# Kernel optimization log

Measured on AMD Instinct MI355X. Metric: run time of the kernel, lower is better.

The kernel has to match this reference:

```python
import jax, jax.numpy as jnp
import numpy as np

B, C, H, W = 8, 512, 32, 32
N = H * W
FG_THRES, BG_THRES, TOPK = 0.7, 0.6, 12


def setup_inputs() -> dict:
    key = jax.random.key(0)
    k1, k2, k3 = jax.random.split(key, 3)
    feature_q = jax.random.normal(k1, (B, C, H, W), dtype=jnp.float32)
    support_feat = jax.random.normal(k2, (B, C, H, W), dtype=jnp.float32)
    support_mask = jax.random.randint(k3, (B, H, W), 0, 2).astype(jnp.int32)
    return {"feature_q": feature_q, "support_feat": support_feat, "support_mask": support_mask}


def _masked_avg_pool(feat, mask):
    # feat [B,C,H,W], mask [B,1,H,W]; interpolate to same size is identity
    return jnp.sum(feat * mask, axis=(2, 3)) / (jnp.sum(mask, axis=(2, 3)) + 1e-5)


def _cosine(a, b):
    # F.cosine_similarity along channel dim 1 (eps=1e-8), with broadcasting
    dot = jnp.sum(a * b, axis=1)
    na = jnp.sqrt(jnp.sum(a * a, axis=1))
    nb = jnp.sqrt(jnp.sum(b * b, axis=1))
    return dot / jnp.maximum(na * nb, 1e-8)


def _similarity(feature_q, fg_proto, bg_proto):
    sim_fg = _cosine(feature_q, fg_proto)
    sim_bg = _cosine(feature_q, bg_proto)
    return jnp.stack([sim_bg, sim_fg], axis=1) * 10.0  # [B,2,H,W]


def _select_weights(pred, thres):
    # pred [N] -> float {0,1} selection weights; threshold mask, topk-12 fallback
    m = pred > thres
    _, top_idx = jax.lax.top_k(pred, TOPK)
    tm = jnp.zeros_like(m).at[top_idx].set(True)
    return jnp.where(m.sum() > 0, m, tm).astype(pred.dtype)


def _ssp_single(cur_feat, pred_fg, pred_bg):
    # cur_feat [C,N]; masked formulation == torch's variable-length column select
    wf = _select_weights(pred_fg, FG_THRES)
    wb = _select_weights(pred_bg, BG_THRES)
    fg_proto = jnp.sum(cur_feat * wf, axis=-1) / wf.sum()  # [C]
    bg_proto = jnp.sum(cur_feat * wb, axis=-1) / wb.sum()
    cn = cur_feat / jnp.sqrt(jnp.sum(cur_feat * cur_feat, axis=0, keepdims=True))
    sim = (cn.T @ cn) * 2.0  # [N,N] cosine sim, scaled
    neg = jnp.asarray(-1e30, sim.dtype)
    fg_attn = jax.nn.softmax(jnp.where(wf[None, :] > 0, sim, neg), axis=-1)
    bg_attn = jax.nn.softmax(jnp.where(wb[None, :] > 0, sim, neg), axis=-1)
    fg_local = (fg_attn @ cur_feat.T).T  # [C,N]
    bg_local = (bg_attn @ cur_feat.T).T
    return fg_proto, bg_proto, fg_local, bg_local


def reference(feature_q, support_feat, support_mask):
    mask_f = (support_mask == 1).astype(feature_q.dtype)[:, None]  # [B,1,H,W]
    mask_b = (support_mask == 0).astype(feature_q.dtype)[:, None]
    FP = _masked_avg_pool(support_feat, mask_f)[:, :, None, None]  # [B,C,1,1]
    BP = _masked_avg_pool(support_feat, mask_b)[:, :, None, None]
    out_0 = _similarity(feature_q, FP, BP)  # [B,2,H,W]
    pred = jax.nn.softmax(out_0, axis=1).reshape(B, 2, N)
    cur = feature_q.reshape(B, C, N)
    fg_p, bg_p, fg_l, bg_l = jax.vmap(_ssp_single)(cur, pred[:, 1], pred[:, 0])
    SSFP = fg_p[:, :, None, None]
    SSBP = bg_p[:, :, None, None]
    ASBP = bg_l.reshape(B, C, H, W)
    FP_1 = FP * 0.5 + SSFP * 0.5
    BP_1 = SSBP * 0.3 + ASBP * 0.7
    out_1 = _similarity(feature_q, FP_1, BP_1)  # [B,2,H,W]
    return out_1
```

## Files before the change

kernel.cpp:

```cpp
#include <hip/hip_runtime.h>
#include <math.h>

#define Bsz 8
#define Cch 512
#define Npx 1024
#define TOPK 12

typedef __attribute__((ext_vector_type(8))) short bf16x8;
typedef __attribute__((ext_vector_type(4))) float f32x4;

__device__ __forceinline__ unsigned short f2bf(float x) {
    unsigned u = __float_as_uint(x);
    u += 0x7FFF + ((u >> 16) & 1);
    return (unsigned short)(u >> 16);
}
__device__ __forceinline__ float bf2f(unsigned short h) {
    return __uint_as_float(((unsigned)h) << 16);
}

__device__ __forceinline__ float warp_sum64(float v) {
    for (int o = 32; o > 0; o >>= 1) v += __shfl_down(v, o);
    return v;
}
__device__ __forceinline__ float block_sum256(float v, float* s4) {
    v = warp_sum64(v);
    int lane = threadIdx.x & 63, w = threadIdx.x >> 6;
    __syncthreads();
    if (lane == 0) s4[w] = v;
    __syncthreads();
    return s4[0] + s4[1] + s4[2] + s4[3];
}
__device__ __forceinline__ float block_sum512(float v, float* s8) {
    v = warp_sum64(v);
    int lane = threadIdx.x & 63, w = threadIdx.x >> 6;
    __syncthreads();
    if (lane == 0) s8[w] = v;
    __syncthreads();
    float r = 0.f;
    #pragma unroll
    for (int k = 0; k < 8; k++) r += s8[k];
    return r;
}

__global__ void k_pool(const float* __restrict__ sf, const int* __restrict__ mask,
                       float* __restrict__ FPo, float* __restrict__ BPo) {
    __shared__ float s4[4];
    int c = blockIdx.x, b = blockIdx.y, t = threadIdx.x;
    const float4* f4 = (const float4*)(sf + ((size_t)b * Cch + c) * Npx);
    const int4* m4 = (const int4*)(mask + (size_t)b * Npx);
    float4 v = f4[t];
    int4 m = m4[t];
    float sumf = (m.x == 1 ? v.x : 0.f) + (m.y == 1 ? v.y : 0.f)
               + (m.z == 1 ? v.z : 0.f) + (m.w == 1 ? v.w : 0.f);
    float tot = v.x + v.y + v.z + v.w;
    float cf = (float)((m.x == 1) + (m.y == 1) + (m.z == 1) + (m.w == 1));
    sumf = block_sum256(sumf, s4);
    tot  = block_sum256(tot, s4);
    cf   = block_sum256(cf, s4);
    if (t == 0) {
        FPo[b * Cch + c] = sumf / (cf + 1e-5f);
        BPo[b * Cch + c] = (tot - sumf) / ((1024.f - cf) + 1e-5f);
    }
}

__global__ void __launch_bounds__(512) k_predcast(const float* __restrict__ fq,
                       const float* __restrict__ FP, const float* __restrict__ BP,
                       float* __restrict__ dsim, float* __restrict__ invn,
                       unsigned short* __restrict__ Ft) {
    __shared__ float sFP[Cch], sBP[Cch], s8[8];
    __shared__ float rdf[16][32], rdb[16][32], rqq[16][32];
    __shared__ unsigned short S[32][522];
    int b = blockIdx.y, t = threadIdx.x;
    int tx = t & 31, ty = t >> 5;
    int p0 = blockIdx.x * 32;
    int p = p0 + tx;
    sFP[t] = FP[b * Cch + t];
    sBP[t] = BP[b * Cch + t];
    __syncthreads();
    float nf = sqrtf(block_sum512(sFP[t] * sFP[t], s8));
    float nb = sqrtf(block_sum512(sBP[t] * sBP[t], s8));
    const float* q = fq + (size_t)b * Cch * Npx + p;
    float df = 0.f, db = 0.f, qq = 0.f;
    int c0 = ty * 32;
    #pragma unroll 4
    for (int c = 0; c < 32; c += 2) {
        float v0 = q[(size_t)(c0 + c) * Npx];
        float v1 = q[(size_t)(c0 + c + 1) * Npx];
        df += v0 * sFP[c0 + c] + v1 * sFP[c0 + c + 1];
        db += v0 * sBP[c0 + c] + v1 * sBP[c0 + c + 1];
        qq += v0 * v0 + v1 * v1;
        unsigned pk = (unsigned)f2bf(v0) | ((unsigned)f2bf(v1) << 16);
        *(unsigned*)&S[tx][c0 + c] = pk;
    }
    rdf[ty][tx] = df; rdb[ty][tx] = db; rqq[ty][tx] = qq;
    __syncthreads();
    for (int s = 8; s > 0; s >>= 1) {
        if (ty < s) {
            rdf[ty][tx] += rdf[ty + s][tx];
            rdb[ty][tx] += rdb[ty + s][tx];
            rqq[ty][tx] += rqq[ty + s][tx];
        }
        __syncthreads();
    }
    if (ty == 0) {
        float nq = sqrtf(rqq[0][tx]);
        float simf = 10.f * rdf[0][tx] / fmaxf(nq * nf, 1e-8f);
        float simb = 10.f * rdb[0][tx] / fmaxf(nq * nb, 1e-8f);
        dsim[b * Npx + p] = simf - simb;
        invn[b * Npx + p] = 1.f / nq;
    }
    int w = t >> 6, lane = t & 63;
    unsigned short* FtB = Ft + (size_t)b * Npx * Cch;
    for (int pr = w; pr < 32; pr += 8) {
        unsigned* dst = (unsigned*)(FtB + (size_t)(p0 + pr) * Cch);
        #pragma unroll
        for (int it = 0; it < 4; it++) {
            int d = it * 64 + lane;
            dst[d] = *(const unsigned*)&S[pr][d * 2];
        }
    }
}

__global__ void __launch_bounds__(1024) k_selcompact(const float* __restrict__ dsim,
                        const float* __restrict__ invn,
                        int* __restrict__ nsf, int* __restrict__ nsb,
                        int* __restrict__ jf, int* __restrict__ jb,
                        float* __restrict__ ivg) {
    __shared__ int wsum[16];
    int b = blockIdx.y, t = threadIdx.x;
    int lane = t & 63, w = t >> 6;
    bool isf = (blockIdx.x == 0);
    float d = dsim[b * Npx + t];
    float key = isf ? d : -d;
    float thres = isf ? 0.8472979f : 0.4054651f;
    int flag = (key > thres) ? 1 : 0;
    int x = flag;
    #pragma unroll
    for (int o = 1; o < 64; o <<= 1) {
        int y = __shfl_up(x, o);
        if (lane >= o) x += y;
    }
    if (lane == 63) wsum[w] = x;
    __syncthreads();
    int base = 0, total = 0;
    #pragma unroll
    for (int k = 0; k < 16; k++) {
        int s = wsum[k];
        if (k < w) base += s;
        total += s;
    }
    if (total == 0) {
        __shared__ int   sc[Npx];
        __shared__ float v[Npx];
        __shared__ float rv[Npx];
        __shared__ int   ri[Npx];
        v[t] = key; flag = 0;
        __syncthreads();
        for (int k = 0; k < TOPK; k++) {
            rv[t] = v[t]; ri[t] = t;
            __syncthreads();
            for (int s = 512; s > 0; s >>= 1) {
                if (t < s) {
                    float a = rv[t], bb = rv[t + s];
                    int ia = ri[t], ib = ri[t + s];
                    if (bb > a || (bb == a && ib < ia)) { rv[t] = bb; ri[t] = ib; }
                }
                __syncthreads();
            }
            int win = ri[0];
            if (t == win) { flag = 1; v[t] = -INFINITY; }
            __syncthreads();
        }
        sc[t] = flag;
        __syncthreads();
        for (int off = 1; off < 1024; off <<= 1) {
            int xx = (t >= off) ? sc[t - off] : 0;
            __syncthreads();
            sc[t] += xx;
            __syncthreads();
        }
        if (flag) {
            int pos = sc[t] - 1;
            if (isf) jf[b * Npx + pos] = t;
            else {
                jb[b * Npx + pos] = t;
                ivg[b * Npx + pos] = invn[b * Npx + t];
            }
        }
        if (t == 1023) { if (isf) nsf[b] = sc[1023]; else nsb[b] = sc[1023]; }
        return;
    }
    if (flag) {
        int pos = base + x - 1;
        if (isf) jf[b * Npx + pos] = t;
        else {
            jb[b * Npx + pos] = t;
            ivg[b * Npx + pos] = invn[b * Npx + t];
        }
    }
    if (t == 0) { if (isf) nsf[b] = total; else nsb[b] = total; }
}

__global__ void k_mid(const float* __restrict__ fq, const unsigned short* __restrict__ Ft,
                      const int* __restrict__ jf, const int* __restrict__ nsf,
                      const int* __restrict__ jb, const int* __restrict__ nsb,
                      unsigned short* __restrict__ Fg,
                      float* __restrict__ fgp, float* __restrict__ bgp) {
    int b = blockIdx.z;
    if (blockIdx.y < 16) {
        int ns = nsb[b];
        int KC = (ns + 31) & ~31;
        int j0 = blockIdx.x * 32;
        if (j0 >= KC) return;
        int c0 = blockIdx.y * 32;
        __shared__ unsigned short tt[32][33];
        int col = threadIdx.x & 31, rr = threadIdx.x >> 5;
        const unsigned short* S = Ft + (size_t)b * Npx * Cch;
        const int* ji = jb + b * Npx;
        for (int r = rr; r < 32; r += 8) {
            int j = j0 + r;
            int src = (j < ns) ? ji[j] : ji[ns - 1];
            tt[r][col] = S[(size_t)src * Cch + c0 + col];
        }
        __syncthreads();
        unsigned short* D = Fg + (size_t)b * Cch * Npx;
        for (int r = rr; r < 32; r += 8)
            D[(size_t)(c0 + r) * Npx + j0 + col] = tt[col][r];
    } else {
        if (blockIdx.x >= 16) return;
        int cb = blockIdx.x * 32;
        int tx = threadIdx.x & 31, ty = threadIdx.x >> 5;
        const float* F = fq + (size_t)b * Cch * Npx;
        for (int which = 0; which < 2; which++) {
            const int* ji = (which ? jb : jf) + b * Npx;
            int ns = (which ? nsb : nsf)[b];
            for (int g = 0; g < 4; g++) {
                int c = cb + g * 8 + ty;
                float s = 0.f;
                for (int k = tx; k < ns; k += 32) s += F[(size_t)c * Npx + ji[k]];
                #pragma unroll
                for (int o = 16; o > 0; o >>= 1) s += __shfl_down(s, o);
                if (tx == 0) (which ? bgp : fgp)[b * Cch + c] = s / (float)ns;
            }
        }
    }
}

__global__ void __launch_bounds__(256) k_gram_c(const unsigned short* __restrict__ Ft,
                                                const int* __restrict__ jb,
                                                const int* __restrict__ nsb,
                                                unsigned short* __restrict__ G) {
    int b = blockIdx.z;
    int ns = nsb[b];
    int KC = (ns + 31) & ~31;
    int j0 = blockIdx.y * 128;
    if (j0 >= KC) return;
    int i0 = blockIdx.x * 128;
    __shared__ unsigned short At[128][40];
    __shared__ unsigned short Bt[128][40];
    __shared__ int sji[128];
    const unsigned short* FA = Ft + (size_t)b * Npx * Cch;
    int tid = threadIdx.x;
    if (tid < 128) {
        int j = j0 + tid;
        sji[tid] = (j < ns) ? jb[b * Npx + j] : jb[b * Npx];
    }
    __syncthreads();
    int l = tid & 63, w = tid >> 6;
    int ml = l & 15, quad = l >> 4;
    int wi = (w & 1) * 64, wj = (w >> 1) * 64;
    f32x4 acc[4][4] = {};
    for (int k0 = 0; k0 < Cch; k0 += 32) {
        #pragma unroll
        for (int s = 0; s < 2; s++) {
            int idx = tid + s * 256;
            int r = idx >> 2, kc = idx & 3;
            *(uint4*)&At[r][kc * 8] = *(const uint4*)(FA + (size_t)(i0 + r) * Cch + k0 + kc * 8);
            *(uint4*)&Bt[r][kc * 8] = *(const uint4*)(FA + (size_t)sji[r] * Cch + k0 + kc * 8);
        }
        __syncthreads();
        bf16x8 af[4], bfr[4];
        #pragma unroll
        for (int u = 0; u < 4; u++) af[u] = *(const bf16x8*)&At[wi + u * 16 + ml][quad * 8];
        #pragma unroll
        for (int v = 0; v < 4; v++) bfr[v] = *(const bf16x8*)&Bt[wj + v * 16 + ml][quad * 8];
        #pragma unroll
        for (int u = 0; u < 4; u++)
            #pragma unroll
            for (int v = 0; v < 4; v++)
                acc[u][v] = __builtin_amdgcn_mfma_f32_16x16x32_bf16(af[u], bfr[v], acc[u][v], 0, 0, 0);
        __syncthreads();
    }
    unsigned short* g = G + (size_t)b * Npx * Npx;
    #pragma unroll
    for (int u = 0; u < 4; u++) {
        int i = i0 + wi + u * 16 + quad * 4;
        #pragma unroll
        for (int v = 0; v < 4; v++) {
            int j = j0 + wj + v * 16 + ml;
            #pragma unroll
            for (int r = 0; r < 4; r++)
                g[(size_t)(i + r) * Npx + j] = f2bf(acc[u][v][r]);
        }
    }
}

__global__ void k_softmax_w(unsigned short* __restrict__ G, const float* __restrict__ invn,
                            const float* __restrict__ ivg, const int* __restrict__ nsb) {
    int b = blockIdx.y;
    int ns = nsb[b];
    int KC = (ns + 31) & ~31;
    int w = threadIdx.x >> 6, l = threadIdx.x & 63;
    int i = blockIdx.x * 4 + w;
    unsigned short* row = G + ((size_t)b * Npx + i) * Npx;
    const float* iv = ivg + (size_t)b * Npx;
    float ivi = 2.f * invn[b * Npx + i];
    float vals[16];
    float sum = 0.f;
    #pragma unroll
    for (int k = 0; k < 16; k++) {
        int jc = k * 64 + l;
        float e = 0.f;
        if (jc < ns) e = expf(bf2f(row[jc]) * ivi * iv[jc]);
        vals[k] = e;
        sum += e;
    }
    #pragma unroll
    for (int o = 32; o > 0; o >>= 1) sum += __shfl_xor(sum, o);
    float inv = 1.f / sum;
    #pragma unroll
    for (int k = 0; k < 16; k++) {
        int jc = k * 64 + l;
        if (jc < KC) row[jc] = f2bf(vals[k] * inv);
    }
}

__global__ void __launch_bounds__(256) k_pv_c(const unsigned short* __restrict__ Fg,
                                              const unsigned short* __restrict__ A,
                                              const int* __restrict__ nsb,
                                              unsigned short* __restrict__ Dout) {
    int b = blockIdx.z;
    int KC = (nsb[b] + 31) & ~31;
    __shared__ unsigned short At[64][40];
    __shared__ unsigned short Bt[128][40];
    int i0 = blockIdx.x * 128, c0 = blockIdx.y * 64;
    const unsigned short* F = Fg + (size_t)b * Cch * Npx;
    const unsigned short* Ar = A + (size_t)b * Npx * Npx;
    int tid = threadIdx.x;
    int l = tid & 63, w = tid >> 6;
    int ml = l & 15, quad = l >> 4;
    int wm = (w & 1) * 32, wn = (w >> 1) * 64;
    f32x4 acc[2][4] = {};
    for (int j0 = 0; j0 < KC; j0 += 32) {
        {
            int r = tid >> 2, kc = tid & 3;
            *(uint4*)&At[r][kc * 8] = *(const uint4*)(F + (size_t)(c0 + r) * Npx + j0 + kc * 8);
        }
        #pragma unroll
        for (int s = 0; s < 2; s++) {
            int idx = tid + s * 256;
            int r = idx >> 2, kc = idx & 3;
            *(uint4*)&Bt[r][kc * 8] = *(const uint4*)(Ar + (size_t)(i0 + r) * Npx + j0 + kc * 8);
        }
        __syncthreads();
        bf16x8 af[2], bfr[4];
        #pragma unroll
        for (int u = 0; u < 2; u++) af[u] = *(const bf16x8*)&At[wm + u * 16 + ml][quad * 8];
        #pragma unroll
        for (int v = 0; v < 4; v++) bfr[v] = *(const bf16x8*)&Bt[wn + v * 16 + ml][quad * 8];
        #pragma unroll
        for (int u = 0; u < 2; u++)
            #pragma unroll
            for (int v = 0; v < 4; v++)
                acc[u][v] = __builtin_amdgcn_mfma_f32_16x16x32_bf16(af[u], bfr[v], acc[u][v], 0, 0, 0);
        __syncthreads();
    }
    unsigned short* D = Dout + (size_t)b * Cch * Npx;
    #pragma unroll
    for (int u = 0; u < 2; u++) {
        int c = c0 + wm + u * 16 + quad * 4;
        #pragma unroll
        for (int v = 0; v < 4; v++) {
            int i = i0 + wn + v * 16 + ml;
            #pragma unroll
            for (int r = 0; r < 4; r++)
                D[(size_t)(c + r) * Npx + i] = f2bf(acc[u][v][r]);
        }
    }
}

__global__ void __launch_bounds__(512) k_out(const unsigned short* __restrict__ Ft,
                      const float* __restrict__ FP,
                      const float* __restrict__ fgp, const float* __restrict__ bgp,
                      const unsigned short* __restrict__ localh, float* __restrict__ out) {
    __shared__ float sFP1[Cch], sBG[Cch], s8[8];
    __shared__ float rdf[16][32], rdb[16][32], rqq[16][32], rnb[16][32];
    int b = blockIdx.y, t = threadIdx.x;
    int tx = t & 31, ty = t >> 5;
    int p = blockIdx.x * 32 + tx;
    sFP1[t] = 0.5f * FP[b * Cch + t] + 0.5f * fgp[b * Cch + t];
    sBG[t] = 0.3f * bgp[b * Cch + t];
    __syncthreads();
    float nf = sqrtf(block_sum512(sFP1[t] * sFP1[t], s8));
    const unsigned short* qr = Ft + ((size_t)b * Npx + p) * Cch;
    const unsigned short* lo = localh + (size_t)b * Cch * Npx + p;
    float df = 0.f, db = 0.f, qq = 0.f, nb2 = 0.f;
    int c0 = ty * 32;
    #pragma unroll
    for (int cc = 0; cc < 4; cc++) {
        bf16x8 qv = *(const bf16x8*)&qr[c0 + cc * 8];
        #pragma unroll
        for (int e = 0; e < 8; e++) {
            int c = c0 + cc * 8 + e;
            float v = bf2f((unsigned short)qv[e]);
            float bp1 = sBG[c] + 0.7f * bf2f(lo[(size_t)c * Npx]);
            df += v * sFP1[c];
            db += v * bp1;
            qq += v * v;
            nb2 += bp1 * bp1;
        }
    }
    rdf[ty][tx] = df; rdb[ty][tx] = db; rqq[ty][tx] = qq; rnb[ty][tx] = nb2;
    __syncthreads();
    for (int s = 8; s > 0; s >>= 1) {
        if (ty < s) {
            rdf[ty][tx] += rdf[ty + s][tx];
            rdb[ty][tx] += rdb[ty + s][tx];
            rqq[ty][tx] += rqq[ty + s][tx];
            rnb[ty][tx] += rnb[ty + s][tx];
        }
        __syncthreads();
    }
    if (ty == 0) {
        float nq = sqrtf(rqq[0][tx]);
        float sf = 10.f * rdf[0][tx] / fmaxf(nq * nf, 1e-8f);
        float sb = 10.f * rdb[0][tx] / fmaxf(nq * sqrtf(rnb[0][tx]), 1e-8f);
        out[((size_t)b * 2) * Npx + p] = sb;
        out[((size_t)b * 2 + 1) * Npx + p] = sf;
    }
}

extern "C" void kernel_launch(void* const* d_in, const int* in_sizes, int n_in,
                              void* d_out, int out_size, void* d_ws, size_t ws_size,
                              hipStream_t stream) {
    const float* fq = (const float*)d_in[0];
    const float* sf = (const float*)d_in[1];
    const int* mask = (const int*)d_in[2];
    float* out = (float*)d_out;

    float* ws = (float*)d_ws;
    float* FP    = ws;
    float* BP    = FP + Bsz * Cch;
    float* fgp   = BP + Bsz * Cch;
    float* bgp   = fgp + Bsz * Cch;
    float* dsim  = bgp + Bsz * Cch;
    float* invn  = dsim + Bsz * Npx;
    float* ivg   = invn + Bsz * Npx;
    int*   nsf   = (int*)(ivg + Bsz * Npx);
    int*   nsb   = nsf + 8;
    int*   jf    = nsb + 8;
    int*   jb    = jf + Bsz * Npx;
    unsigned short* Ft     = (unsigned short*)(jb + Bsz * Npx);
    unsigned short* Fg     = Ft + (size_t)Bsz * Npx * Cch;
    unsigned short* Gb     = Fg + (size_t)Bsz * Cch * Npx;
    unsigned short* localh = Gb + (size_t)Bsz * Npx * Npx;

    k_pool<<<dim3(Cch, Bsz), 256, 0, stream>>>(sf, mask, FP, BP);
    k_predcast<<<dim3(Npx / 32, Bsz), 512, 0, stream>>>(fq, FP, BP, dsim, invn, Ft);
    k_selcompact<<<dim3(2, Bsz), 1024, 0, stream>>>(dsim, invn, nsf, nsb, jf, jb, ivg);
    k_mid<<<dim3(32, 17, Bsz), 256, 0, stream>>>(fq, Ft, jf, nsf, jb, nsb, Fg, fgp, bgp);
    k_gram_c<<<dim3(8, 8, Bsz), 256, 0, stream>>>(Ft, jb, nsb, Gb);
    k_softmax_w<<<dim3(Npx / 4, Bsz), 256, 0, stream>>>(Gb, invn, ivg, nsb);
    k_pv_c<<<dim3(8, 8, Bsz), 256, 0, stream>>>(Fg, Gb, nsb, localh);
    k_out<<<dim3(Npx / 32, Bsz), 512, 0, stream>>>(Ft, FP, fgp, bgp, localh, out);
}
```

Measured before the change: 153.3 us.

## Fuse softmax exponent into gram GEMM epilogue, defer normalization to PV kernel

The separate softmax kernel is removed. The gram GEMM epilogue now computes the exponentiated cosine scores directly, writes them as bf16, and atomically accumulates per-row denominators into a buffer that k_predcast zeroes. The PV GEMM divides by these denominators in its epilogue. Both GEMMs gain register-prefetch double buffering of the next K tile, and the gram tile shrinks to 128x64 to double the grid. This removes a full read-modify-write pass over the NxN matrix and one launch, at the cost of atomics and a softmax with no max subtraction, which is safe only because the scaled cosine values are bounded.

```diff
diff --git a/kernel.cpp b/kernel.cpp
--- a/kernel.cpp
+++ b/kernel.cpp
@@ -66,7 +66,7 @@
 __global__ void __launch_bounds__(512) k_predcast(const float* __restrict__ fq,
                        const float* __restrict__ FP, const float* __restrict__ BP,
                        float* __restrict__ dsim, float* __restrict__ invn,
-                       unsigned short* __restrict__ Ft) {
+                       unsigned short* __restrict__ Ft, float* __restrict__ denom) {
     __shared__ float sFP[Cch], sBP[Cch], s8[8];
     __shared__ float rdf[16][32], rdb[16][32], rqq[16][32];
     __shared__ unsigned short S[32][522];
@@ -74,6 +74,7 @@
     int tx = t & 31, ty = t >> 5;
     int p0 = blockIdx.x * 32;
     int p = p0 + tx;
+    if (t < 32) denom[b * Npx + p0 + t] = 0.f;
     sFP[t] = FP[b * Cch + t];
     sBP[t] = BP[b * Cch + t];
     __syncthreads();
@@ -246,98 +247,93 @@
     }
 }
 
-__global__ void __launch_bounds__(256) k_gram_c(const unsigned short* __restrict__ Ft,
-                                                const int* __restrict__ jb,
-                                                const int* __restrict__ nsb,
-                                                unsigned short* __restrict__ G) {
+__global__ void __launch_bounds__(256) k_gram_fused(const unsigned short* __restrict__ Ft,
+                        const int* __restrict__ jb, const int* __restrict__ nsb,
+                        const float* __restrict__ invn, const float* __restrict__ ivg,
+                        unsigned short* __restrict__ G, float* __restrict__ denom) {
     int b = blockIdx.z;
     int ns = nsb[b];
     int KC = (ns + 31) & ~31;
-    int j0 = blockIdx.y * 128;
+    int j0 = blockIdx.y * 64;
     if (j0 >= KC) return;
     int i0 = blockIdx.x * 128;
     __shared__ unsigned short At[128][40];
-    __shared__ unsigned short Bt[128][40];
-    __shared__ int sji[128];
+    __shared__ unsigned short Bt[64][40];
+    __shared__ int sji[64];
+    __shared__ float sfi[128], sfj[64];
     const unsigned short* FA = Ft + (size_t)b * Npx * Cch;
     int tid = threadIdx.x;
-    if (tid < 128) {
+    if (tid < 64) {
         int j = j0 + tid;
         sji[tid] = (j < ns) ? jb[b * Npx + j] : jb[b * Npx];
-    }
-    __syncthreads();
+        sfj[tid] = (j < ns) ? ivg[b * Npx + j] : 0.f;
+    }
+    if (tid < 128) sfi[tid] = 2.f * invn[b * Npx + i0 + tid];
+    __syncthreads();
+    int rA = tid >> 2, kc8 = (tid & 3) * 8;
+    const unsigned short* sa0 = FA + (size_t)(i0 + rA) * Cch + kc8;
+    const unsigned short* sa1 = sa0 + (size_t)64 * Cch;
+    const unsigned short* sb0 = FA + (size_t)sji[rA] * Cch + kc8;
+    unsigned short* wa0 = &At[rA][kc8];
+    unsigned short* wa1 = &At[64 + rA][kc8];
+    unsigned short* wb0 = &Bt[rA][kc8];
     int l = tid & 63, w = tid >> 6;
     int ml = l & 15, quad = l >> 4;
-    int wi = (w & 1) * 64, wj = (w >> 1) * 64;
-    f32x4 acc[4][4] = {};
+    int wi = (w & 1) * 64, wj = (w >> 1) * 32;
+    f32x4 acc[4][2] = {};
+    uint4 a0 = *(const uint4*)sa0;
+    uint4 a1 = *(const uint4*)sa1;
+    uint4 b0 = *(const uint4*)sb0;
     for (int k0 = 0; k0 < Cch; k0 += 32) {
-        #pragma unroll
-        for (int s = 0; s < 2; s++) {
-            int idx = tid + s * 256;
-            int r = idx >> 2, kc = idx & 3;
-            *(uint4*)&At[r][kc * 8] = *(const uint4*)(FA + (size_t)(i0 + r) * Cch + k0 + kc * 8);
-            *(uint4*)&Bt[r][kc * 8] = *(const uint4*)(FA + (size_t)sji[r] * Cch + k0 + kc * 8);
-        }
-        __syncthreads();
-        bf16x8 af[4], bfr[4];
+        __syncthreads();
+        *(uint4*)wa0 = a0; *(uint4*)wa1 = a1; *(uint4*)wb0 = b0;
+        __syncthreads();
+        int kn = k0 + 32;
+        if (kn < Cch) {
+            a0 = *(const uint4*)(sa0 + kn);
+            a1 = *(const uint4*)(sa1 + kn);
+            b0 = *(const uint4*)(sb0 + kn);
+        }
+        bf16x8 af[4], bfr[2];
         #pragma unroll
         for (int u = 0; u < 4; u++) af[u] = *(const bf16x8*)&At[wi + u * 16 + ml][quad * 8];
         #pragma unroll
-        for (int v = 0; v < 4; v++) bfr[v] = *(const bf16x8*)&Bt[wj + v * 16 + ml][quad * 8];
+        for (int v = 0; v < 2; v++) bfr[v] = *(const bf16x8*)&Bt[wj + v * 16 + ml][quad * 8];
         #pragma unroll
         for (int u = 0; u < 4; u++)
             #pragma unroll
-            for (int v = 0; v < 4; v++)
+            for (int v = 0; v < 2; v++)
                 acc[u][v] = __builtin_amdgcn_mfma_f32_16x16x32_bf16(af[u], bfr[v], acc[u][v], 0, 0, 0);
-        __syncthreads();
     }
     unsigned short* g = G + (size_t)b * Npx * Npx;
+    float* dn = denom + b * Npx;
     #pragma unroll
     for (int u = 0; u < 4; u++) {
-        int i = i0 + wi + u * 16 + quad * 4;
-        #pragma unroll
-        for (int v = 0; v < 4; v++) {
-            int j = j0 + wj + v * 16 + ml;
+        int il = wi + u * 16 + quad * 4;
+        #pragma unroll
+        for (int r = 0; r < 4; r++) {
+            float fi = sfi[il + r];
+            float s = 0.f;
             #pragma unroll
-            for (int r = 0; r < 4; r++)
-                g[(size_t)(i + r) * Npx + j] = f2bf(acc[u][v][r]);
-        }
-    }
-}
-
-__global__ void k_softmax_w(unsigned short* __restrict__ G, const float* __restrict__ invn,
-                            const float* __restrict__ ivg, const int* __restrict__ nsb) {
-    int b = blockIdx.y;
-    int ns = nsb[b];
-    int KC = (ns + 31) & ~31;
-    int w = threadIdx.x >> 6, l = threadIdx.x & 63;
-    int i = blockIdx.x * 4 + w;
-    unsigned short* row = G + ((size_t)b * Npx + i) * Npx;
-    const float* iv = ivg + (size_t)b * Npx;
-    float ivi = 2.f * invn[b * Npx + i];
-    float vals[16];
-    float sum = 0.f;
-    #pragma unroll
-    for (int k = 0; k < 16; k++) {
-        int jc = k * 64 + l;
-        float e = 0.f;
-        if (jc < ns) e = expf(bf2f(row[jc]) * ivi * iv[jc]);
-        vals[k] = e;
-        sum += e;
-    }
-    #pragma unroll
-    for (int o = 32; o > 0; o >>= 1) sum += __shfl_xor(sum, o);
-    float inv = 1.f / sum;
-    #pragma unroll
-    for (int k = 0; k < 16; k++) {
-        int jc = k * 64 + l;
-        if (jc < KC) row[jc] = f2bf(vals[k] * inv);
+            for (int v = 0; v < 2; v++) {
+                int jl = wj + v * 16 + ml;
+                float e = 0.f;
+                if (j0 + jl < ns) e = expf(acc[u][v][r] * fi * sfj[jl]);
+                unsigned short eb = f2bf(e);
+                g[(size_t)(i0 + il + r) * Npx + j0 + jl] = eb;
+                s += bf2f(eb);
+            }
+            #pragma unroll
+            for (int m = 1; m < 16; m <<= 1) s += __shfl_xor(s, m);
+            if (ml == 0) atomicAdd(&dn[i0 + il + r], s);
+        }
     }
 }
 
 __global__ void __launch_bounds__(256) k_pv_c(const unsigned short* __restrict__ Fg,
                                               const unsigned short* __restrict__ A,
                                               const int* __restrict__ nsb,
+                                              const float* __restrict__ denom,
                                               unsigned short* __restrict__ Dout) {
     int b = blockIdx.z;
     int KC = (nsb[b] + 31) & ~31;
@@ -347,22 +343,30 @@
     const unsigned short* F = Fg + (size_t)b * Cch * Npx;
     const unsigned short* Ar = A + (size_t)b * Npx * Npx;
     int tid = threadIdx.x;
+    int rr = tid >> 2, kc8 = (tid & 3) * 8;
+    const unsigned short* sa0 = F + (size_t)(c0 + rr) * Npx + kc8;
+    const unsigned short* sb0 = Ar + (size_t)(i0 + rr) * Npx + kc8;
+    const unsigned short* sb1 = sb0 + (size_t)64 * Npx;
+    unsigned short* wa0 = &At[rr][kc8];
+    unsigned short* wb0 = &Bt[rr][kc8];
+    unsigned short* wb1 = &Bt[64 + rr][kc8];
     int l = tid & 63, w = tid >> 6;
     int ml = l & 15, quad = l >> 4;
     int wm = (w & 1) * 32, wn = (w >> 1) * 64;
     f32x4 acc[2][4] = {};
+    uint4 a0 = *(const uint4*)sa0;
+    uint4 b0 = *(const uint4*)sb0;
+    uint4 b1 = *(const uint4*)sb1;
     for (int j0 = 0; j0 < KC; j0 += 32) {
-        {
-            int r = tid >> 2, kc = tid & 3;
-            *(uint4*)&At[r][kc * 8] = *(const uint4*)(F + (size_t)(c0 + r) * Npx + j0 + kc * 8);
-        }
-        #pragma unroll
-        for (int s = 0; s < 2; s++) {
-            int idx = tid + s * 256;
-            int r = idx >> 2, kc = idx & 3;
-            *(uint4*)&Bt[r][kc * 8] = *(const uint4*)(Ar + (size_t)(i0 + r) * Npx + j0 + kc * 8);
-        }
-        __syncthreads();
+        __syncthreads();
+        *(uint4*)wa0 = a0; *(uint4*)wb0 = b0; *(uint4*)wb1 = b1;
+        __syncthreads();
+        int jn = j0 + 32;
+        if (jn < KC) {
+            a0 = *(const uint4*)(sa0 + jn);
+            b0 = *(const uint4*)(sb0 + jn);
+            b1 = *(const uint4*)(sb1 + jn);
+        }
         bf16x8 af[2], bfr[4];
         #pragma unroll
         for (int u = 0; u < 2; u++) af[u] = *(const bf16x8*)&At[wm + u * 16 + ml][quad * 8];
@@ -373,8 +377,10 @@
             #pragma unroll
             for (int v = 0; v < 4; v++)
                 acc[u][v] = __builtin_amdgcn_mfma_f32_16x16x32_bf16(af[u], bfr[v], acc[u][v], 0, 0, 0);
-        __syncthreads();
-    }
+    }
+    float rd[4];
+    #pragma unroll
+    for (int v = 0; v < 4; v++) rd[v] = 1.f / denom[b * Npx + i0 + wn + v * 16 + ml];
     unsigned short* D = Dout + (size_t)b * Cch * Npx;
     #pragma unroll
     for (int u = 0; u < 2; u++) {
@@ -384,7 +390,7 @@
             int i = i0 + wn + v * 16 + ml;
             #pragma unroll
             for (int r = 0; r < 4; r++)
-                D[(size_t)(c + r) * Npx + i] = f2bf(acc[u][v][r]);
+                D[(size_t)(c + r) * Npx + i] = f2bf(acc[u][v][r] * rd[v]);
         }
     }
 }
@@ -464,13 +470,13 @@
     unsigned short* Fg     = Ft + (size_t)Bsz * Npx * Cch;
     unsigned short* Gb     = Fg + (size_t)Bsz * Cch * Npx;
     unsigned short* localh = Gb + (size_t)Bsz * Npx * Npx;
+    float* denom = (float*)(localh + (size_t)Bsz * Cch * Npx);
 
     k_pool<<<dim3(Cch, Bsz), 256, 0, stream>>>(sf, mask, FP, BP);
-    k_predcast<<<dim3(Npx / 32, Bsz), 512, 0, stream>>>(fq, FP, BP, dsim, invn, Ft);
+    k_predcast<<<dim3(Npx / 32, Bsz), 512, 0, stream>>>(fq, FP, BP, dsim, invn, Ft, denom);
     k_selcompact<<<dim3(2, Bsz), 1024, 0, stream>>>(dsim, invn, nsf, nsb, jf, jb, ivg);
     k_mid<<<dim3(32, 17, Bsz), 256, 0, stream>>>(fq, Ft, jf, nsf, jb, nsb, Fg, fgp, bgp);
-    k_gram_c<<<dim3(8, 8, Bsz), 256, 0, stream>>>(Ft, jb, nsb, Gb);
-    k_softmax_w<<<dim3(Npx / 4, Bsz), 256, 0, stream>>>(Gb, invn, ivg, nsb);
-    k_pv_c<<<dim3(8, 8, Bsz), 256, 0, stream>>>(Fg, Gb, nsb, localh);
+    k_gram_fused<<<dim3(8, 16, Bsz), 256, 0, stream>>>(Ft, jb, nsb, invn, ivg, Gb, denom);
+    k_pv_c<<<dim3(8, 8, Bsz), 256, 0, stream>>>(Fg, Gb, nsb, denom, localh);
     k_out<<<dim3(Npx / 32, Bsz), 512, 0, stream>>>(Ft, FP, fgp, bgp, localh, out);
 }
```

Measured after the change: 153.8 us. Within noise of the previous version (+0.3%).
